# Kernel optimization log

Hardware: AMD Instinct MI355X
Metric: run time of the kernel (lower is better)

## Reference

```python
import jax, jax.numpy as jnp
import numpy as np

B, F, C, H, W = 16, 256, 64, 64, 64   # batch, features, z_channels(e_dim), height, width
N_E = 512                              # codebooksize
BETA = 1.0
EPS = 1e-5


def setup_inputs() -> dict:
    key = jax.random.key(0)
    ks = jax.random.split(key, 4)
    x = jax.random.normal(ks[0], (B, F, H, W), jnp.float32)
    emb = jax.random.normal(ks[1], (N_E, C), jnp.float32)
    emb = emb / jnp.linalg.norm(emb, axis=1, keepdims=True)  # points on hypersphere
    return dict(
        x=x,
        bn1_gamma=jnp.ones((F,), jnp.float32),
        bn1_beta=jnp.zeros((F,), jnp.float32),
        conv1_w=jax.random.normal(ks[2], (C, F), jnp.float32) * np.float32(1.0 / np.sqrt(F)),
        conv1_b=jnp.zeros((C,), jnp.float32),
        conv2_w=jax.random.normal(ks[3], (C, C), jnp.float32) * np.float32(1.0 / np.sqrt(C)),
        conv2_b=jnp.zeros((C,), jnp.float32),
        embedding=emb,
        r=jnp.ones((N_E,), jnp.float32),
    )


def reference(x, bn1_gamma, bn1_beta, conv1_w, conv1_b, conv2_w, conv2_b, embedding, r):
    sg = jax.lax.stop_gradient
    # BatchNorm2d (training mode: batch stats, biased variance)
    mu = x.mean(axis=(0, 2, 3), keepdims=True)
    var = x.var(axis=(0, 2, 3), keepdims=True)
    x1 = (x - mu) * jax.lax.rsqrt(var + EPS)
    x1 = x1 * bn1_gamma[None, :, None, None] + bn1_beta[None, :, None, None]
    # 1x1 convs (note: original overwrites norm2 output, conv2 consumes conv1 output directly)
    x1 = jnp.einsum('bfhw,cf->bchw', x1, conv1_w) + conv1_b[None, :, None, None]
    z = jnp.einsum('bchw,oc->bohw', x1, conv2_w) + conv2_b[None, :, None, None]

    zf = z.reshape(-1, C)  # [B*C*H*W/e_dim view == flat rows of e_dim]
    # codebook angular statistics (norms detached, as torch.Tensor(list) detaches)
    d1 = embedding @ embedding.T                                 # [n_e, n_e]
    en = sg(jnp.linalg.norm(embedding, axis=1))                  # [n_e]
    edx = jnp.clip(d1 / (en[:, None] * en[None, :]), -0.99999, 0.99999)
    ang = jnp.arccos(edx)
    total_min_distance = jnp.mean(jnp.sort(ang, axis=0)[1])      # kthvalue(.,2,dim=0)
    codebookvariance = jnp.mean(jnp.var(ang, axis=1, ddof=1))    # torch.var unbiased

    # VQ dispatch: squared L2 distances + argmin + gather
    d = (zf ** 2).sum(1, keepdims=True) + (embedding ** 2).sum(1) - 2.0 * (zf @ embedding.T)
    idx = jnp.argmin(d, axis=1)                                  # [ntok]
    z_q = embedding[idx].reshape(z.shape)

    hsw = jnp.mean(jnp.square(r - en))
    # legacy=True path with beta=1.0, ignorezq=False, disentangle=True
    loss = jnp.mean((sg(z_q) - z) ** 2) + BETA * jnp.mean((z_q - sg(z)) ** 2)
    loss = loss + hsw + (codebookvariance - total_min_distance)

    z_q = z + sg(z_q - z)  # straight-through
    cb_loss = jnp.float32(0.0)  # prev_cb is None
    r_c = r + sg(jnp.clip(r, 0.9, 1.1) - r)  # Clamp with straight-through grad
    mean_r = jnp.mean(r_c)
    return (loss, z_q, codebookvariance, total_min_distance, hsw, cb_loss, mean_r)
```

## Files before the change

kernel.cpp:

```cpp
#include <hip/hip_runtime.h>
#include <math.h>


#define CAP    2048
#define MARGIN 4e-3f

#define WS_WHI  0
#define WS_WLO  8192
#define WS_BP   16384
#define WS_EN   16448
#define WS_E2   16960
#define WS_ACC  17472
#define WS_CNT  17480
#define WS_WL   17488
#define WS_EFT  19536
#define WS_WD   52304
#define WS_BPD  85072
#define WS_PART 85200
#define WS_EHI  87248
#define WS_ELO  103632

typedef __attribute__((ext_vector_type(8))) __bf16 bf16v8;
typedef __attribute__((ext_vector_type(4))) float  f32v4;

__device__ __forceinline__ unsigned short f2bf(float f) {
    union { float f; unsigned u; } v; v.f = f;
    unsigned r = v.u + 0x7FFFu + ((v.u >> 16) & 1u);
    return (unsigned short)(r >> 16);
}
__device__ __forceinline__ float bf2f(unsigned short h) {
    union { unsigned u; float f; } v; v.u = ((unsigned)h) << 16; return v.f;
}
__device__ __forceinline__ void load_lds16(const float* g, unsigned* l) {
    __builtin_amdgcn_global_load_lds((const __attribute__((address_space(1))) void*)g,
                                     (__attribute__((address_space(3))) void*)l, 16, 0, 0);
}

__global__ __launch_bounds__(256) void bn_partial(
    const float* __restrict__ x, double* __restrict__ part)
{
    const int f = blockIdx.x >> 1, ch = blockIdx.x & 1, t = threadIdx.x;
    double s = 0.0, q = 0.0;
    #pragma unroll 1
    for (int bb = 0; bb < 8; ++bb) {
        const int b = ch * 8 + bb;
        const float4* p = (const float4*)(x + ((size_t)(b * 256 + f) << 12));
        #pragma unroll
        for (int ii = 0; ii < 4; ++ii) {
            float4 u = p[t + ii * 256];
            double dx = u.x, dy = u.y, dz = u.z, dw = u.w;
            s += (dx + dy) + (dz + dw);
            q = fma(dx, dx, q); q = fma(dy, dy, q);
            q = fma(dz, dz, q); q = fma(dw, dw, q);
        }
    }
    #pragma unroll
    for (int off = 32; off; off >>= 1) { s += __shfl_xor(s, off, 64); q += __shfl_xor(q, off, 64); }
    __shared__ double sh[8];
    const int wv = t >> 6;
    if ((t & 63) == 0) { sh[wv * 2] = s; sh[wv * 2 + 1] = q; }
    __syncthreads();
    if (t == 0) {
        part[blockIdx.x * 2]     = (sh[0] + sh[2]) + (sh[4] + sh[6]);
        part[blockIdx.x * 2 + 1] = (sh[1] + sh[3]) + (sh[5] + sh[7]);
    }
}

__global__ __launch_bounds__(256) void prep(
    const float* __restrict__ w1, const float* __restrict__ w2,
    const float* __restrict__ b1, const float* __restrict__ b2,
    const float* __restrict__ gamma, const float* __restrict__ beta,
    const float* __restrict__ emb, const double* __restrict__ part,
    unsigned short* __restrict__ whi, unsigned short* __restrict__ wlo,
    double* __restrict__ Wd,
    double* __restrict__ bpd, float* __restrict__ bp,
    float* __restrict__ eft, float* __restrict__ en, float* __restrict__ e2,
    unsigned short* __restrict__ ehi, unsigned short* __restrict__ elo,
    float* __restrict__ accs, int* __restrict__ cnt)
{
    __shared__ double sh_ad[4];
    __shared__ double cdl[256];
    __shared__ double red[4][64];
    __shared__ double tsh[64];
    const int t = threadIdx.x;

    if (blockIdx.x < 64) {
        const int o = t & 63, fi = t >> 6;
        const int f = blockIdx.x * 4 + fi;
        if (o == 0) {
            double s = part[(2 * f) * 2]     + part[(2 * f + 1) * 2];
            double q = part[(2 * f) * 2 + 1] + part[(2 * f + 1) * 2 + 1];
            double mean = s * (1.0 / 65536.0);
            double var  = q * (1.0 / 65536.0) - mean * mean;
            sh_ad[fi] = (double)gamma[f] / sqrt(var + 1e-5);
        }
        __syncthreads();
        double s = 0.0;
        for (int c = 0; c < 64; ++c)
            s = fma((double)w2[o * 64 + c], (double)w1[c * 256 + f], s);
        double wp = s * sh_ad[fi];
        Wd[o * 256 + f] = wp;
        {
            float wpf = (float)wp;
            unsigned short wh = f2bf(wpf);
            unsigned short wlv = f2bf(wpf - bf2f(wh));
            int mt = o >> 4, cq_ = o & 15, sK = f >> 5, qd_ = (f >> 3) & 3, j = f & 7;
            int idx = ((mt * 8 + sK) * 64 + qd_ * 16 + cq_) * 8 + j;
            whi[idx] = wh; wlo[idx] = wlv;
        }

        const int lane = t & 63, wv = t >> 6;
        #pragma unroll
        for (int rr = 0; rr < 2; ++rr) {
            int n = blockIdx.x * 8 + rr * 4 + wv;
            float v = emb[n * 64 + lane];
            eft[lane * 512 + n] = v;
            unsigned short hb = f2bf(v);
            unsigned short lb = f2bf(v - bf2f(hb));
            int pos = (lane >> 3) ^ (n & 7);
            ehi[n * 64 + pos * 8 + (lane & 7)] = hb;
            elo[n * 64 + pos * 8 + (lane & 7)] = lb;
            float qq = v * v;
            #pragma unroll
            for (int off = 32; off; off >>= 1) qq += __shfl_xor(qq, off, 64);
            if (lane == 0) { e2[n] = qq; en[n] = sqrtf(qq); }
        }
    } else {
        {
            const int f = t;
            double s = part[(2 * f) * 2]     + part[(2 * f + 1) * 2];
            double q = part[(2 * f) * 2 + 1] + part[(2 * f + 1) * 2 + 1];
            double mean = s * (1.0 / 65536.0);
            double var  = q * (1.0 / 65536.0) - mean * mean;
            double a = (double)gamma[f] / sqrt(var + 1e-5);
            cdl[f] = (double)beta[f] - mean * a;
        }
        __syncthreads();
        const int o = t & 63, p = t >> 6;
        double ss = 0.0;
        for (int j = 0; j < 64; ++j) {
            int fidx = p * 64 + j;
            ss = fma((double)w1[o * 256 + fidx], cdl[fidx], ss);
        }
        red[p][o] = ss; __syncthreads();
        if (t < 64) tsh[t] = (double)b1[t] + (red[0][t] + red[1][t]) + (red[2][t] + red[3][t]);
        __syncthreads();
        if (t < 64) {
            double bb = (double)b2[t];
            for (int c = 0; c < 64; ++c)
                bb = fma((double)w2[t * 64 + c], tsh[c], bb);
            bpd[t] = bb;
            bp[t]  = (float)bb;
        }
        if (t < 8) accs[t] = 0.f;
        if (t == 0) cnt[0] = 0;
    }
}

__global__ __launch_bounds__(256, 2) void fused_gemm_vq(
    const float* __restrict__ x,
    const unsigned short* __restrict__ whi,
    const unsigned short* __restrict__ wlo,
    const float* __restrict__ bp,
    const float* __restrict__ emb,
    const float* __restrict__ e2,
    const float* __restrict__ en,
    const float* __restrict__ eft,
    const unsigned short* __restrict__ ehi,
    const unsigned short* __restrict__ elo,
    float* __restrict__ accs,
    int* __restrict__ cnt, int* __restrict__ wl,
    float* __restrict__ zq)
{
    __shared__ __align__(16) unsigned smem[4880];
    enum { OAR = 0,
           OE2 = 4096, OZ2 = 4608, ODT = 4672, OD2T = 4736, OIT = 4800 };
    float* e2s = (float*)(smem + OE2);
    float* z2s = (float*)(smem + OZ2);
    float* dT  = (float*)(smem + ODT);
    float* d2T = (float*)(smem + OD2T);
    int*   iT  = (int*)(smem + OIT);

    const int tid = threadIdx.x, lane = tid & 63, wv = tid >> 6;

    if (blockIdx.x >= 1024) {
        const int i = blockIdx.x - 1024;
        float* ang = e2s;
        const float eni = en[i];
        const float* ei = emb + (i << 6);
        #pragma unroll
        for (int jj = 0; jj < 2; ++jj) {
            const int j = tid + jj * 256;
            float d0 = 0.f, d1 = 0.f, d2 = 0.f, d3 = 0.f;
            #pragma unroll
            for (int k = 0; k < 64; k += 4) {
                d0 = fmaf(ei[k + 0], eft[(k + 0) * 512 + j], d0);
                d1 = fmaf(ei[k + 1], eft[(k + 1) * 512 + j], d1);
                d2 = fmaf(ei[k + 2], eft[(k + 2) * 512 + j], d2);
                d3 = fmaf(ei[k + 3], eft[(k + 3) * 512 + j], d3);
            }
            float dot = (d0 + d1) + (d2 + d3);
            float xv = dot / (eni * en[j]);
            xv = fminf(fmaxf(xv, -0.99999f), 0.99999f);
            ang[j] = acosf(xv);
        }
        __syncthreads();
        if (wv == 0) {
            float m1 = 3.4e38f, m2 = 3.4e38f, ssum = 0.f;
            #pragma unroll
            for (int t8 = 0; t8 < 8; ++t8) {
                float a = ang[t8 * 64 + lane];
                ssum += a;
                if (a < m1) { m2 = m1; m1 = a; }
                else if (a < m2) m2 = a;
            }
            #pragma unroll
            for (int off = 32; off; off >>= 1) ssum += __shfl_xor(ssum, off, 64);
            #pragma unroll
            for (int off = 32; off; off >>= 1) {
                float o1 = __shfl_xor(m1, off, 64);
                float o2 = __shfl_xor(m2, off, 64);
                if (o1 < m1) { m2 = fminf(m1, o2); m1 = o1; }
                else          m2 = fminf(m2, o1);
            }
            float mean = ssum * (1.f / 512.f);
            float vs = 0.f;
            #pragma unroll
            for (int t8 = 0; t8 < 8; ++t8) {
                float tt = ang[t8 * 64 + lane] - mean;
                vs = fmaf(tt, tt, vs);
            }
            #pragma unroll
            for (int off = 32; off; off >>= 1) vs += __shfl_xor(vs, off, 64);
            if (lane == 0) {
                atomicAdd(accs + 1, vs * (1.f / 511.f));
                atomicAdd(accs + 2, m2);
            }
        }
        return;
    }

    const int wvu = __builtin_amdgcn_readfirstlane(wv);
    const int b = blockIdx.x >> 6, h = blockIdx.x & 63;
    const int cq = lane & 15, qd = lane >> 4;

    bf16v8 Ahi[8], Alo[8];
    #pragma unroll
    for (int s = 0; s < 8; ++s) {
        Ahi[s] = *(const bf16v8*)(whi + ((size_t)((wvu * 8 + s) * 64 + lane)) * 8);
        Alo[s] = *(const bf16v8*)(wlo + ((size_t)((wvu * 8 + s) * 64 + lane)) * 8);
    }
    e2s[tid]       = e2[tid];
    e2s[tid + 256] = e2[tid + 256];

    const float* xb = x + ((size_t)(b * 256 + wvu * 16) << 12) + (h << 6) + lane;
    float xv[16];
    #pragma unroll
    for (int i = 0; i < 16; ++i) xv[i] = xb[(size_t)i << 12];

    f32v4 acc[4];
    #pragma unroll
    for (int nt = 0; nt < 4; ++nt) acc[nt] = (f32v4){0.f, 0.f, 0.f, 0.f};

    #pragma unroll
    for (int chk = 0; chk < 4; ++chk) {
        __syncthreads();
        #pragma unroll
        for (int p = 0; p < 8; ++p) {
            const int i = 2 * p;
            unsigned short h0 = f2bf(xv[i]),     h1 = f2bf(xv[i + 1]);
            unsigned short l0 = f2bf(xv[i] - bf2f(h0));
            unsigned short l1 = f2bf(xv[i + 1] - bf2f(h1));
            const int g = 2 * wvu + (p >> 2);
            const int widx = lane * 32 + ((g ^ (lane & 7)) << 2) + (p & 3);
            smem[OAR + widx]        = (unsigned)h0 | ((unsigned)h1 << 16);
            smem[OAR + 2048 + widx] = (unsigned)l0 | ((unsigned)l1 << 16);
        }
        __syncthreads();
        if (chk < 3) {
            const float* xb2 = xb + ((size_t)((chk + 1) * 64) << 12);
            #pragma unroll
            for (int i = 0; i < 16; ++i) xv[i] = xb2[(size_t)i << 12];
        }
        #pragma unroll
        for (int st2 = 0; st2 < 2; ++st2) {
            const int s = chk * 2 + st2;
            #pragma unroll
            for (int nt = 0; nt < 4; ++nt) {
                const int row = nt * 16 + cq;
                const int pos = row * 32 + (((st2 * 4 + qd) ^ (row & 7)) << 2);
                bf16v8 bh = *(const bf16v8*)(smem + OAR + pos);
                bf16v8 bl = *(const bf16v8*)(smem + OAR + 2048 + pos);
                acc[nt] = __builtin_amdgcn_mfma_f32_16x16x32_bf16(Ahi[s], bh, acc[nt], 0, 0, 0);
                acc[nt] = __builtin_amdgcn_mfma_f32_16x16x32_bf16(Ahi[s], bl, acc[nt], 0, 0, 0);
                acc[nt] = __builtin_amdgcn_mfma_f32_16x16x32_bf16(Alo[s], bh, acc[nt], 0, 0, 0);
            }
        }
    }
    __syncthreads();

    float zvr[4][4];
    {
        float bpv[4];
        #pragma unroll
        for (int r = 0; r < 4; ++r) bpv[r] = bp[wvu * 16 + qd * 4 + r];
        #pragma unroll
        for (int nt = 0; nt < 4; ++nt)
            #pragma unroll
            for (int r = 0; r < 4; ++r) zvr[nt][r] = acc[nt][r] + bpv[r];
        float z2p[4];
        #pragma unroll
        for (int r = 0; r < 4; ++r) {
            float p2 = 0.f;
            #pragma unroll
            for (int nt = 0; nt < 4; ++nt) p2 = fmaf(zvr[nt][r], zvr[nt][r], p2);
            #pragma unroll
            for (int off = 1; off <= 8; off <<= 1) p2 += __shfl_xor(p2, off, 64);
            z2p[r] = p2;
        }
        if (cq == 0) {
            #pragma unroll
            for (int r = 0; r < 4; ++r) z2s[wvu * 16 + qd * 4 + r] = z2p[r];
        }
        unsigned short* ar = (unsigned short*)(smem + OAR);
        #pragma unroll
        for (int nt = 0; nt < 4; ++nt) {
            const int w = nt * 16 + cq;
            const int gz = w >> 3, kj = w & 7;
            #pragma unroll
            for (int r = 0; r < 4; ++r) {
                const int tok = wvu * 16 + qd * 4 + r;
                const int hw = tok * 64 + ((gz ^ (tok & 7)) << 3) + kj;
                unsigned short zh = f2bf(zvr[nt][r]);
                ar[hw]        = zh;
                ar[4096 + hw] = f2bf(zvr[nt][r] - bf2f(zh));
            }
        }
    }
    __syncthreads();

    const int x7 = cq & 7;
    bf16v8 vahi[2], valo[2];
    {
        const int rbase = (wvu * 16 + cq) * 32;
        #pragma unroll
        for (int s = 0; s < 2; ++s) {
            int pos = ((s * 4 + qd) ^ x7) * 4;
            vahi[s] = *(const bf16v8*)(smem + OAR + rbase + pos);
            valo[s] = *(const bf16v8*)(smem + OAR + 2048 + rbase + pos);
        }
    }
    __syncthreads();

    if (wvu == 0) {
        const float* gh = (const float*)ehi;
        const float* gl = (const float*)elo;
        #pragma unroll
        for (int j = 0; j < 4; ++j) load_lds16(gh + j * 256 + lane * 4, smem + OAR + j * 256);
        #pragma unroll
        for (int j = 0; j < 4; ++j) load_lds16(gl + j * 256 + lane * 4, smem + OAR + 1024 + j * 256);
        gh += 1024; gl += 1024;
        #pragma unroll
        for (int j = 0; j < 4; ++j) load_lds16(gh + j * 256 + lane * 4, smem + OAR + 2048 + j * 256);
        #pragma unroll
        for (int j = 0; j < 4; ++j) load_lds16(gl + j * 256 + lane * 4, smem + OAR + 3072 + j * 256);
    }

    float z2r[4];
    float m1[4] = {3.4e38f, 3.4e38f, 3.4e38f, 3.4e38f};
    float m2[4] = {3.4e38f, 3.4e38f, 3.4e38f, 3.4e38f};
    int   i1[4] = {0, 0, 0, 0};
    const int p0 = (qd ^ x7) * 4, p1 = ((4 + qd) ^ x7) * 4;

    #pragma unroll 1
    for (int t2 = 0; t2 < 32; ++t2) {
        if ((t2 & 1) == 0) {
            __syncthreads();
            int st = t2 >> 1;
            if (wvu == 0 && st < 15) {
                const float* gh = (const float*)ehi + (size_t)(st + 1) * 1024;
                const float* gl = (const float*)elo + (size_t)(st + 1) * 1024;
                unsigned* dst = smem + OAR + ((st + 1) & 1) * 2048;
                #pragma unroll
                for (int j = 0; j < 4; ++j) load_lds16(gh + j * 256 + lane * 4, dst + j * 256);
                #pragma unroll
                for (int j = 0; j < 4; ++j) load_lds16(gl + j * 256 + lane * 4, dst + 1024 + j * 256);
            }
            if (t2 == 0) {
                #pragma unroll
                for (int r = 0; r < 4; ++r) z2r[r] = z2s[wvu * 16 + qd * 4 + r];
            }
        }
        const int rb = OAR + ((t2 >> 1) & 1) * 2048 + ((t2 & 1) * 16 + cq) * 32;
        bf16v8 bh0 = *(const bf16v8*)(smem + rb + p0);
        bf16v8 bh1 = *(const bf16v8*)(smem + rb + p1);
        bf16v8 bl0 = *(const bf16v8*)(smem + rb + 1024 + p0);
        bf16v8 bl1 = *(const bf16v8*)(smem + rb + 1024 + p1);
        f32v4 a0 = {0.f, 0.f, 0.f, 0.f}, a1 = {0.f, 0.f, 0.f, 0.f};
        a0 = __builtin_amdgcn_mfma_f32_16x16x32_bf16(vahi[0], bh0, a0, 0, 0, 0);
        a1 = __builtin_amdgcn_mfma_f32_16x16x32_bf16(vahi[1], bh1, a1, 0, 0, 0);
        a0 = __builtin_amdgcn_mfma_f32_16x16x32_bf16(vahi[0], bl0, a0, 0, 0, 0);
        a1 = __builtin_amdgcn_mfma_f32_16x16x32_bf16(vahi[1], bl1, a1, 0, 0, 0);
        a0 = __builtin_amdgcn_mfma_f32_16x16x32_bf16(valo[0], bh0, a0, 0, 0, 0);
        a1 = __builtin_amdgcn_mfma_f32_16x16x32_bf16(valo[1], bh1, a1, 0, 0, 0);
        a0 = __builtin_amdgcn_mfma_f32_16x16x32_bf16(valo[0], bl0, a0, 0, 0, 0);
        a1 = __builtin_amdgcn_mfma_f32_16x16x32_bf16(valo[1], bl1, a1, 0, 0, 0);
        const float eps = e2s[t2 * 16 + cq];
        const int n = t2 * 16 + cq;
        #pragma unroll
        for (int r = 0; r < 4; ++r) {
            float d = fmaf(-2.f, a0[r] + a1[r], z2r[r] + eps);
            if (d < m1[r])      { m2[r] = m1[r]; m1[r] = d; i1[r] = n; }
            else if (d < m2[r]) { m2[r] = d; }
        }
    }

    #pragma unroll
    for (int r = 0; r < 4; ++r) {
        #pragma unroll
        for (int off = 1; off <= 8; off <<= 1) {
            float o1 = __shfl_xor(m1[r], off, 64);
            float o2 = __shfl_xor(m2[r], off, 64);
            int   oi = __shfl_xor(i1[r], off, 64);
            if (o1 < m1[r] || (o1 == m1[r] && oi < i1[r])) {
                m2[r] = fminf(m1[r], o2); m1[r] = o1; i1[r] = oi;
            } else {
                m2[r] = fminf(m2[r], o1);
            }
        }
    }
    if (cq == 0) {
        #pragma unroll
        for (int r = 0; r < 4; ++r) {
            int tok = wvu * 16 + qd * 4 + r;
            dT[tok] = m1[r]; d2T[tok] = m2[r]; iT[tok] = i1[r];
        }
    }
    __syncthreads();

    if (wv == 0) {
        float mm1 = dT[lane], mm2 = d2T[lane];
        if (mm2 - mm1 < MARGIN) {
            int pos = atomicAdd(cnt, 1);
            if (pos < CAP) wl[pos] = ((b << 6) + lane) * 64 + h;
        }
        float ms = mm1;
        #pragma unroll
        for (int off = 32; off; off >>= 1) ms += __shfl_xor(ms, off, 64);
        if (lane == 0) atomicAdd(accs + 0, ms);
    }
    __syncthreads();

    float* zrow = zq + ((size_t)(b * 64) << 12) + (h << 6) + lane;
    #pragma unroll
    for (int cc = 0; cc < 16; ++cc) {
        int c = wvu * 16 + cc;
        int id = iT[c];
        zrow[(size_t)c << 12] = emb[(id << 6) + lane];
    }
}

__global__ __launch_bounds__(256) void refine_fin(
    const float* __restrict__ x,
    const double* __restrict__ Wd,
    const double* __restrict__ bpd,
    const float* __restrict__ emb,
    const float* __restrict__ eft,
    const int* __restrict__ cnt, const int* __restrict__ wl,
    float* __restrict__ zq,
    const float* __restrict__ accs, const float* __restrict__ en,
    const float* __restrict__ r, float* __restrict__ out)
{
    const int tid = threadIdx.x, lane = tid & 63, wv = tid >> 6;

    if (blockIdx.x == 256) {
        if (wv == 0) {
            float hs = 0.f, rs = 0.f;
            #pragma unroll
            for (int jj = 0; jj < 8; ++jj) {
                int n = (jj << 6) + lane;
                float rv = r[n];
                float d = rv - en[n];
                hs = fmaf(d, d, hs);
                rs += fminf(fmaxf(rv, 0.9f), 1.1f);
            }
            #pragma unroll
            for (int off = 32; off; off >>= 1) { hs += __shfl_xor(hs, off, 64); rs += __shfl_xor(rs, off, 64); }
            if (lane == 0) {
                float hsw    = hs * (1.f / 512.f);
                float mean_r = rs * (1.f / 512.f);
                float mse    = accs[0] * (1.f / 4194304.f);
                float cbv    = accs[1] * (1.f / 512.f);
                float tmd    = accs[2] * (1.f / 512.f);
                float loss   = 2.f * mse + hsw + (cbv - tmd);
                out[0]       = loss;
                out[4194305] = cbv;
                out[4194306] = tmd;
                out[4194307] = hsw;
                out[4194308] = 0.f;
                out[4194309] = mean_r;
            }
        }
        return;
    }

    int count = cnt[0]; if (count > CAP) count = CAP;

    __shared__ double zp[4][64];
    __shared__ double zs[64];
    __shared__ double dsh[256];
    __shared__ int    ish[256];

    for (int it = blockIdx.x; it < count; it += 256) {
        const int r2 = wl[it];
        const int b = r2 >> 12, c = (r2 >> 6) & 63, h = r2 & 63;

        const float* xp = x + (((size_t)(b * 256 + wv * 64)) << 12) + (h << 6) + lane;
        const double* wrow = Wd + c * 256 + wv * 64;
        double zd = 0.0;
        #pragma unroll 8
        for (int f = 0; f < 64; ++f)
            zd = fma(wrow[f], (double)xp[((size_t)f) << 12], zd);
        zp[wv][lane] = zd;
        __syncthreads();
        if (tid < 64) zs[tid] = (zp[0][tid] + zp[1][tid]) + (zp[2][tid] + zp[3][tid]) + bpd[c];
        __syncthreads();

        double dm = 1e300; int im = 0;
        #pragma unroll
        for (int jj = 0; jj < 2; ++jj) {
            int n = (jj << 8) + tid;
            double d = 0.0;
            #pragma unroll 8
            for (int k = 0; k < 64; ++k) {
                double t = zs[k] - (double)eft[(k << 9) + n];
                d = fma(t, t, d);
            }
            if (d < dm) { dm = d; im = n; }
        }
        dsh[tid] = dm; ish[tid] = im;
        __syncthreads();
        for (int st = 128; st; st >>= 1) {
            if (tid < st) {
                double od = dsh[tid + st]; int oi = ish[tid + st];
                if (od < dsh[tid] || (od == dsh[tid] && oi < ish[tid])) { dsh[tid] = od; ish[tid] = oi; }
            }
            __syncthreads();
        }
        if (tid < 64) {
            int idx = ish[0];
            zq[((size_t)r2 << 6) + tid] = emb[(idx << 6) + tid];
        }
        __syncthreads();
    }
}

extern "C" void kernel_launch(void* const* d_in, const int* in_sizes, int n_in,
                              void* d_out, int out_size, void* d_ws, size_t ws_size,
                              hipStream_t stream) {
    const float* x   = (const float*)d_in[0];
    const float* g1  = (const float*)d_in[1];
    const float* be1 = (const float*)d_in[2];
    const float* w1  = (const float*)d_in[3];
    const float* b1  = (const float*)d_in[4];
    const float* w2  = (const float*)d_in[5];
    const float* b2  = (const float*)d_in[6];
    const float* emb = (const float*)d_in[7];
    const float* r   = (const float*)d_in[8];
    float* ws = (float*)d_ws;
    float* out = (float*)d_out;

    double* WD   = (double*)(ws + WS_WD);
    double* BPD  = (double*)(ws + WS_BPD);
    double* PART = (double*)(ws + WS_PART);
    int*    CNT  = (int*)(ws + WS_CNT);
    int*    WL   = (int*)(ws + WS_WL);
    unsigned short* WHI = (unsigned short*)(ws + WS_WHI);
    unsigned short* WLO = (unsigned short*)(ws + WS_WLO);
    unsigned short* EHI = (unsigned short*)(ws + WS_EHI);
    unsigned short* ELO = (unsigned short*)(ws + WS_ELO);

    bn_partial<<<512, 256, 0, stream>>>(x, PART);
    prep<<<65, 256, 0, stream>>>(w1, w2, b1, b2, g1, be1, emb, PART,
                                 WHI, WLO, WD, BPD, ws + WS_BP,
                                 ws + WS_EFT, ws + WS_EN, ws + WS_E2,
                                 EHI, ELO, ws + WS_ACC, CNT);
    fused_gemm_vq<<<1536, 256, 0, stream>>>(x, WHI, WLO, ws + WS_BP,
                                            emb, ws + WS_E2, ws + WS_EN, ws + WS_EFT,
                                            EHI, ELO, ws + WS_ACC, CNT, WL, out + 1);
    refine_fin<<<257, 256, 0, stream>>>(x, WD, BPD, emb, ws + WS_EFT, CNT, WL,
                                        out + 1, ws + WS_ACC, ws + WS_EN, r, out);
}
```

Before: 197.8 us.

## Trim VQ distance MFMAs, vectorize bf16 split stores, spread codebook loads across waves

Makes several independent changes to the main VQ kernel. Bias is folded into the accumulator init, and bf16 conversion now uses hardware casts with 128-bit LDS stores. The distance loop switches to one accumulator with six MFMAs, dropping the lo*lo term, and runs a branchless max-score argmax. Codebook LDS prefetch is split across all four waves instead of wave 0 alone. The refine kernel gets multiple FP64 accumulators for more ILP. Dropping the lo*lo term and changing the rounding path could shift near-tie decisions, which the margin-based refine pass is meant to catch.

Result: faster. 185.9 us (-6.0%).

```diff
diff --git a/kernel.cpp b/kernel.cpp
--- a/kernel.cpp
+++ b/kernel.cpp
@@ -21,15 +21,23 @@
 #define WS_ELO  103632
 
 typedef __attribute__((ext_vector_type(8))) __bf16 bf16v8;
+typedef __attribute__((ext_vector_type(2))) __bf16 bf16v2;
 typedef __attribute__((ext_vector_type(4))) float  f32v4;
+typedef __attribute__((ext_vector_type(4))) unsigned u32v4;
 
 __device__ __forceinline__ unsigned short f2bf(float f) {
-    union { float f; unsigned u; } v; v.f = f;
-    unsigned r = v.u + 0x7FFFu + ((v.u >> 16) & 1u);
-    return (unsigned short)(r >> 16);
+    __bf16 h = (__bf16)f;
+    return __builtin_bit_cast(unsigned short, h);
 }
 __device__ __forceinline__ float bf2f(unsigned short h) {
     union { unsigned u; float f; } v; v.u = ((unsigned)h) << 16; return v.f;
+}
+__device__ __forceinline__ unsigned pack_bf2(float a, float b) {
+    bf16v2 v = { (__bf16)a, (__bf16)b };
+    return __builtin_bit_cast(unsigned, v);
+}
+__device__ __forceinline__ float bfhi(float a) {
+    return (float)(__bf16)a;
 }
 __device__ __forceinline__ void load_lds16(const float* g, unsigned* l) {
     __builtin_amdgcn_global_load_lds((const __attribute__((address_space(1))) void*)g,
@@ -250,6 +258,9 @@
         Ahi[s] = *(const bf16v8*)(whi + ((size_t)((wvu * 8 + s) * 64 + lane)) * 8);
         Alo[s] = *(const bf16v8*)(wlo + ((size_t)((wvu * 8 + s) * 64 + lane)) * 8);
     }
+    float bpv[4];
+    #pragma unroll
+    for (int r = 0; r < 4; ++r) bpv[r] = bp[wvu * 16 + qd * 4 + r];
     e2s[tid]       = e2[tid];
     e2s[tid + 256] = e2[tid + 256];
 
@@ -260,21 +271,25 @@
 
     f32v4 acc[4];
     #pragma unroll
-    for (int nt = 0; nt < 4; ++nt) acc[nt] = (f32v4){0.f, 0.f, 0.f, 0.f};
+    for (int nt = 0; nt < 4; ++nt) acc[nt] = (f32v4){bpv[0], bpv[1], bpv[2], bpv[3]};
 
     #pragma unroll
     for (int chk = 0; chk < 4; ++chk) {
         __syncthreads();
-        #pragma unroll
-        for (int p = 0; p < 8; ++p) {
-            const int i = 2 * p;
-            unsigned short h0 = f2bf(xv[i]),     h1 = f2bf(xv[i + 1]);
-            unsigned short l0 = f2bf(xv[i] - bf2f(h0));
-            unsigned short l1 = f2bf(xv[i + 1] - bf2f(h1));
-            const int g = 2 * wvu + (p >> 2);
-            const int widx = lane * 32 + ((g ^ (lane & 7)) << 2) + (p & 3);
-            smem[OAR + widx]        = (unsigned)h0 | ((unsigned)h1 << 16);
-            smem[OAR + 2048 + widx] = (unsigned)l0 | ((unsigned)l1 << 16);
+        {
+            unsigned hb[8], lb[8];
+            #pragma unroll
+            for (int p = 0; p < 8; ++p) {
+                float a = xv[2 * p], bq = xv[2 * p + 1];
+                hb[p] = pack_bf2(a, bq);
+                lb[p] = pack_bf2(a - bfhi(a), bq - bfhi(bq));
+            }
+            const int b0 = lane * 32 + (((2 * wvu) ^ (lane & 7)) << 2);
+            const int b1 = lane * 32 + (((2 * wvu + 1) ^ (lane & 7)) << 2);
+            *(u32v4*)(smem + OAR + b0)        = (u32v4){hb[0], hb[1], hb[2], hb[3]};
+            *(u32v4*)(smem + OAR + b1)        = (u32v4){hb[4], hb[5], hb[6], hb[7]};
+            *(u32v4*)(smem + OAR + 2048 + b0) = (u32v4){lb[0], lb[1], lb[2], lb[3]};
+            *(u32v4*)(smem + OAR + 2048 + b1) = (u32v4){lb[4], lb[5], lb[6], lb[7]};
         }
         __syncthreads();
         if (chk < 3) {
@@ -299,21 +314,13 @@
     }
     __syncthreads();
 
-    float zvr[4][4];
     {
-        float bpv[4];
-        #pragma unroll
-        for (int r = 0; r < 4; ++r) bpv[r] = bp[wvu * 16 + qd * 4 + r];
-        #pragma unroll
-        for (int nt = 0; nt < 4; ++nt)
-            #pragma unroll
-            for (int r = 0; r < 4; ++r) zvr[nt][r] = acc[nt][r] + bpv[r];
         float z2p[4];
         #pragma unroll
         for (int r = 0; r < 4; ++r) {
             float p2 = 0.f;
             #pragma unroll
-            for (int nt = 0; nt < 4; ++nt) p2 = fmaf(zvr[nt][r], zvr[nt][r], p2);
+            for (int nt = 0; nt < 4; ++nt) p2 = fmaf(acc[nt][r], acc[nt][r], p2);
             #pragma unroll
             for (int off = 1; off <= 8; off <<= 1) p2 += __shfl_xor(p2, off, 64);
             z2p[r] = p2;
@@ -331,9 +338,9 @@
             for (int r = 0; r < 4; ++r) {
                 const int tok = wvu * 16 + qd * 4 + r;
                 const int hw = tok * 64 + ((gz ^ (tok & 7)) << 3) + kj;
-                unsigned short zh = f2bf(zvr[nt][r]);
+                unsigned short zh = f2bf(acc[nt][r]);
                 ar[hw]        = zh;
-                ar[4096 + hw] = f2bf(zvr[nt][r] - bf2f(zh));
+                ar[4096 + hw] = f2bf(acc[nt][r] - bf2f(zh));
             }
         }
     }
@@ -352,23 +359,17 @@
     }
     __syncthreads();
 
-    if (wvu == 0) {
+    {
         const float* gh = (const float*)ehi;
         const float* gl = (const float*)elo;
-        #pragma unroll
-        for (int j = 0; j < 4; ++j) load_lds16(gh + j * 256 + lane * 4, smem + OAR + j * 256);
-        #pragma unroll
-        for (int j = 0; j < 4; ++j) load_lds16(gl + j * 256 + lane * 4, smem + OAR + 1024 + j * 256);
-        gh += 1024; gl += 1024;
-        #pragma unroll
-        for (int j = 0; j < 4; ++j) load_lds16(gh + j * 256 + lane * 4, smem + OAR + 2048 + j * 256);
-        #pragma unroll
-        for (int j = 0; j < 4; ++j) load_lds16(gl + j * 256 + lane * 4, smem + OAR + 3072 + j * 256);
-    }
-
-    float z2r[4];
-    float m1[4] = {3.4e38f, 3.4e38f, 3.4e38f, 3.4e38f};
-    float m2[4] = {3.4e38f, 3.4e38f, 3.4e38f, 3.4e38f};
+        load_lds16(gh + wvu * 256 + lane * 4,        smem + OAR + wvu * 256);
+        load_lds16(gl + wvu * 256 + lane * 4,        smem + OAR + 1024 + wvu * 256);
+        load_lds16(gh + 1024 + wvu * 256 + lane * 4, smem + OAR + 2048 + wvu * 256);
+        load_lds16(gl + 1024 + wvu * 256 + lane * 4, smem + OAR + 3072 + wvu * 256);
+    }
+
+    float m1[4] = {-3.4e38f, -3.4e38f, -3.4e38f, -3.4e38f};
+    float m2[4] = {-3.4e38f, -3.4e38f, -3.4e38f, -3.4e38f};
     int   i1[4] = {0, 0, 0, 0};
     const int p0 = (qd ^ x7) * 4, p1 = ((4 + qd) ^ x7) * 4;
 
@@ -377,18 +378,12 @@
         if ((t2 & 1) == 0) {
             __syncthreads();
             int st = t2 >> 1;
-            if (wvu == 0 && st < 15) {
+            if (st >= 1 && st < 15) {
                 const float* gh = (const float*)ehi + (size_t)(st + 1) * 1024;
                 const float* gl = (const float*)elo + (size_t)(st + 1) * 1024;
                 unsigned* dst = smem + OAR + ((st + 1) & 1) * 2048;
-                #pragma unroll
-                for (int j = 0; j < 4; ++j) load_lds16(gh + j * 256 + lane * 4, dst + j * 256);
-                #pragma unroll
-                for (int j = 0; j < 4; ++j) load_lds16(gl + j * 256 + lane * 4, dst + 1024 + j * 256);
-            }
-            if (t2 == 0) {
-                #pragma unroll
-                for (int r = 0; r < 4; ++r) z2r[r] = z2s[wvu * 16 + qd * 4 + r];
+                load_lds16(gh + wvu * 256 + lane * 4, dst + wvu * 256);
+                load_lds16(gl + wvu * 256 + lane * 4, dst + 1024 + wvu * 256);
             }
         }
         const int rb = OAR + ((t2 >> 1) & 1) * 2048 + ((t2 & 1) * 16 + cq) * 32;
@@ -396,22 +391,24 @@
         bf16v8 bh1 = *(const bf16v8*)(smem + rb + p1);
         bf16v8 bl0 = *(const bf16v8*)(smem + rb + 1024 + p0);
         bf16v8 bl1 = *(const bf16v8*)(smem + rb + 1024 + p1);
-        f32v4 a0 = {0.f, 0.f, 0.f, 0.f}, a1 = {0.f, 0.f, 0.f, 0.f};
-        a0 = __builtin_amdgcn_mfma_f32_16x16x32_bf16(vahi[0], bh0, a0, 0, 0, 0);
-        a1 = __builtin_amdgcn_mfma_f32_16x16x32_bf16(vahi[1], bh1, a1, 0, 0, 0);
-        a0 = __builtin_amdgcn_mfma_f32_16x16x32_bf16(vahi[0], bl0, a0, 0, 0, 0);
-        a1 = __builtin_amdgcn_mfma_f32_16x16x32_bf16(vahi[1], bl1, a1, 0, 0, 0);
-        a0 = __builtin_amdgcn_mfma_f32_16x16x32_bf16(valo[0], bh0, a0, 0, 0, 0);
-        a1 = __builtin_amdgcn_mfma_f32_16x16x32_bf16(valo[1], bh1, a1, 0, 0, 0);
-        a0 = __builtin_amdgcn_mfma_f32_16x16x32_bf16(valo[0], bl0, a0, 0, 0, 0);
-        a1 = __builtin_amdgcn_mfma_f32_16x16x32_bf16(valo[1], bl1, a1, 0, 0, 0);
         const float eps = e2s[t2 * 16 + cq];
+        f32v4 a = {0.f, 0.f, 0.f, 0.f};
+        __builtin_amdgcn_s_setprio(1);
+        a = __builtin_amdgcn_mfma_f32_16x16x32_bf16(vahi[0], bh0, a, 0, 0, 0);
+        a = __builtin_amdgcn_mfma_f32_16x16x32_bf16(vahi[1], bh1, a, 0, 0, 0);
+        a = __builtin_amdgcn_mfma_f32_16x16x32_bf16(vahi[0], bl0, a, 0, 0, 0);
+        a = __builtin_amdgcn_mfma_f32_16x16x32_bf16(vahi[1], bl1, a, 0, 0, 0);
+        a = __builtin_amdgcn_mfma_f32_16x16x32_bf16(valo[0], bh0, a, 0, 0, 0);
+        a = __builtin_amdgcn_mfma_f32_16x16x32_bf16(valo[1], bh1, a, 0, 0, 0);
+        __builtin_amdgcn_s_setprio(0);
         const int n = t2 * 16 + cq;
         #pragma unroll
         for (int r = 0; r < 4; ++r) {
-            float d = fmaf(-2.f, a0[r] + a1[r], z2r[r] + eps);
-            if (d < m1[r])      { m2[r] = m1[r]; m1[r] = d; i1[r] = n; }
-            else if (d < m2[r]) { m2[r] = d; }
+            float s = fmaf(-0.5f, eps, a[r]);
+            bool gt = s > m1[r];
+            m2[r] = fminf(fmaxf(s, m2[r]), m1[r]);
+            i1[r] = gt ? n : i1[r];
+            m1[r] = fmaxf(s, m1[r]);
         }
     }
 
@@ -422,10 +419,10 @@
             float o1 = __shfl_xor(m1[r], off, 64);
             float o2 = __shfl_xor(m2[r], off, 64);
             int   oi = __shfl_xor(i1[r], off, 64);
-            if (o1 < m1[r] || (o1 == m1[r] && oi < i1[r])) {
-                m2[r] = fminf(m1[r], o2); m1[r] = o1; i1[r] = oi;
+            if (o1 > m1[r] || (o1 == m1[r] && oi < i1[r])) {
+                m2[r] = fmaxf(m1[r], o2); m1[r] = o1; i1[r] = oi;
             } else {
-                m2[r] = fminf(m2[r], o1);
+                m2[r] = fmaxf(m2[r], o1);
             }
         }
     }
@@ -439,12 +436,12 @@
     __syncthreads();
 
     if (wv == 0) {
-        float mm1 = dT[lane], mm2 = d2T[lane];
-        if (mm2 - mm1 < MARGIN) {
+        float s1 = dT[lane], s2 = d2T[lane];
+        if (s1 - s2 < MARGIN * 0.5f) {
             int pos = atomicAdd(cnt, 1);
             if (pos < CAP) wl[pos] = ((b << 6) + lane) * 64 + h;
         }
-        float ms = mm1;
+        float ms = z2s[lane] - 2.f * s1;
         #pragma unroll
         for (int off = 32; off; off >>= 1) ms += __shfl_xor(ms, off, 64);
         if (lane == 0) atomicAdd(accs + 0, ms);
@@ -517,11 +514,19 @@
 
         const float* xp = x + (((size_t)(b * 256 + wv * 64)) << 12) + (h << 6) + lane;
         const double* wrow = Wd + c * 256 + wv * 64;
-        double zd = 0.0;
-        #pragma unroll 8
-        for (int f = 0; f < 64; ++f)
-            zd = fma(wrow[f], (double)xp[((size_t)f) << 12], zd);
-        zp[wv][lane] = zd;
+        double z0 = 0.0, z1 = 0.0, z2a = 0.0, z3 = 0.0;
+        #pragma unroll
+        for (int f = 0; f < 64; f += 4) {
+            float a0 = xp[(size_t)(f + 0) << 12];
+            float a1 = xp[(size_t)(f + 1) << 12];
+            float a2 = xp[(size_t)(f + 2) << 12];
+            float a3 = xp[(size_t)(f + 3) << 12];
+            z0  = fma(wrow[f + 0], (double)a0, z0);
+            z1  = fma(wrow[f + 1], (double)a1, z1);
+            z2a = fma(wrow[f + 2], (double)a2, z2a);
+            z3  = fma(wrow[f + 3], (double)a3, z3);
+        }
+        zp[wv][lane] = (z0 + z1) + (z2a + z3);
         __syncthreads();
         if (tid < 64) zs[tid] = (zp[0][tid] + zp[1][tid]) + (zp[2][tid] + zp[3][tid]) + bpd[c];
         __syncthreads();
@@ -530,12 +535,14 @@
         #pragma unroll
         for (int jj = 0; jj < 2; ++jj) {
             int n = (jj << 8) + tid;
-            double d = 0.0;
+            double da = 0.0, db = 0.0;
             #pragma unroll 8
-            for (int k = 0; k < 64; ++k) {
-                double t = zs[k] - (double)eft[(k << 9) + n];
-                d = fma(t, t, d);
-            }
+            for (int k = 0; k < 64; k += 2) {
+                double t0 = zs[k]     - (double)eft[(k << 9) + n];
+                double t1 = zs[k + 1] - (double)eft[((k + 1) << 9) + n];
+                da = fma(t0, t0, da); db = fma(t1, t1, db);
+            }
+            double d = da + db;
             if (d < dm) { dm = d; im = n; }
         }
         dsh[tid] = dm; ish[tid] = im;
```
